# Kernel tuning notes

Measured on AMD Instinct MI355X. Metric: run time of the kernel, lower is better.

Reference implementation:

```python
import jax, jax.numpy as jnp
import numpy as np

MASK_FILL = -99999.0  # value used by masked_fill_ in the torch source


def setup_inputs() -> dict:
    key = jax.random.key(0)
    k1, k2, k3, k4, k5, k6, k7 = jax.random.split(key, 7)
    B, S, H = 8, 2048, 1024
    query = jax.random.normal(k1, (B, S, H), dtype=jnp.float32)
    key_t = jax.random.normal(k2, (B, S, H), dtype=jnp.float32)
    value = jax.random.normal(k3, (B, S, H), dtype=jnp.float32)
    mask = jax.random.randint(k4, (B, S), 0, 2, dtype=jnp.int32)
    s = 1.0 / np.sqrt(H)
    Wq = jax.random.uniform(k5, (H, H), dtype=jnp.float32, minval=-s, maxval=s)
    Wk = jax.random.uniform(k6, (H, H), dtype=jnp.float32, minval=-s, maxval=s)
    Wv = jax.random.uniform(k7, (H, H), dtype=jnp.float32, minval=-s, maxval=s)
    return {"query": query, "key": key_t, "value": value,
            "Wq": Wq, "Wk": Wk, "Wv": Wv, "mask": mask}


def reference(query, key, value, Wq, Wk, Wv, mask):
    # Linear(h,h,bias=False): y = x @ W.T
    q = jnp.einsum('bsh,oh->bso', query, Wq)
    k = jnp.einsum('bsh,oh->bso', key, Wk)
    v = jnp.einsum('bsh,oh->bso', value, Wv)
    # score[b,i,j] = q[b,i,:] . k[b,j,:]  (NO 1/sqrt(d) scaling in source)
    score = jnp.einsum('bqh,bkh->bqk', q, k)
    # mask: [B, S_k] -> [B, 1, S_k]; positions where mask==0 get MASK_FILL
    m = mask[:, None, :]
    score = jnp.where(m == 0, jnp.float32(MASK_FILL), score)
    attn = jax.nn.softmax(score, axis=-1)
    context = jnp.einsum('bqk,bkh->bqh', attn, v)
    return context
```

## Files before the change

kernel.cpp:

```cpp
#include <hip/hip_runtime.h>
#include <hip/hip_fp16.h>
#include <math.h>

typedef _Float16 f16;
typedef _Float16 f16x4 __attribute__((ext_vector_type(4)));
typedef _Float16 f16x8 __attribute__((ext_vector_type(8)));
typedef float f32x4 __attribute__((ext_vector_type(4)));
typedef float f32x4e __attribute__((ext_vector_type(4)));

#define GLOAD_LDS16(g, l)                                                                  \
    __builtin_amdgcn_global_load_lds((const __attribute__((address_space(1))) void*)(g),   \
                                     (__attribute__((address_space(3))) void*)(l), 16, 0, 0)

__global__ __launch_bounds__(256) void cast3_kernel(const float* __restrict__ s0,
                                                    const float* __restrict__ s1,
                                                    const float* __restrict__ s2,
                                                    f16* d0, f16* d1, f16* d2, int n16each)
{
    const int z = blockIdx.z;
    const float* src = (z == 0) ? s0 : (z == 1) ? s1 : s2;
    f16* dst = (z == 0) ? d0 : (z == 1) ? d1 : d2;
    const int stride = gridDim.x * blockDim.x;
    for (int i = blockIdx.x * blockDim.x + threadIdx.x; i < n16each; i += stride) {
        const f32x4e* sp = (const f32x4e*)(src + (long long)i * 16);
        f32x4e a = __builtin_nontemporal_load(sp + 0);
        f32x4e b = __builtin_nontemporal_load(sp + 1);
        f32x4e c = __builtin_nontemporal_load(sp + 2);
        f32x4e d4 = __builtin_nontemporal_load(sp + 3);
        f16x8 lo = {(f16)a[0], (f16)a[1], (f16)a[2], (f16)a[3],
                    (f16)b[0], (f16)b[1], (f16)b[2], (f16)b[3]};
        f16x8 hi = {(f16)c[0], (f16)c[1], (f16)c[2], (f16)c[3],
                    (f16)d4[0], (f16)d4[1], (f16)d4[2], (f16)d4[3]};
        f16x8* dp = (f16x8*)(dst + (long long)i * 16);
        dp[0] = lo;
        dp[1] = hi;
    }
}

__global__ __launch_bounds__(256) void transcast_w_kernel(const float* __restrict__ Wq,
                                                          const float* __restrict__ Wk,
                                                          f16* __restrict__ dA,
                                                          f16* __restrict__ dB)
{
    __shared__ f16 tile[64][72];
    const float* src = blockIdx.z ? Wk : Wq;
    f16* dst = blockIdx.z ? dB : dA;
    const int h0 = blockIdx.x * 64, o0 = blockIdx.y * 64;
    const int t = threadIdx.x;
    const int r = t >> 2, c = (t & 3) * 16;
    const float* sp = src + (long long)(o0 + r) * 1024 + h0 + c;
    float4 v0 = *(const float4*)(sp + 0);
    float4 v1 = *(const float4*)(sp + 4);
    float4 v2 = *(const float4*)(sp + 8);
    float4 v3 = *(const float4*)(sp + 12);
    *(f16x4*)&tile[r][c]      = (f16x4){(f16)v0.x, (f16)v0.y, (f16)v0.z, (f16)v0.w};
    *(f16x4*)&tile[r][c + 4]  = (f16x4){(f16)v1.x, (f16)v1.y, (f16)v1.z, (f16)v1.w};
    *(f16x4*)&tile[r][c + 8]  = (f16x4){(f16)v2.x, (f16)v2.y, (f16)v2.z, (f16)v2.w};
    *(f16x4*)&tile[r][c + 12] = (f16x4){(f16)v3.x, (f16)v3.y, (f16)v3.z, (f16)v3.w};
    __syncthreads();
    f16 buf[16];
#pragma unroll
    for (int j = 0; j < 16; j++) buf[j] = tile[c + j][r];
    f16* dp = dst + (long long)(h0 + r) * 1024 + o0 + c;
    *(f16x8*)(dp)     = *(f16x8*)&buf[0];
    *(f16x8*)(dp + 8) = *(f16x8*)&buf[8];
}

template <int OUTF16, int TRANSC>
__global__ __launch_bounds__(512, 2) void gemm_nt_k(
    const f16* __restrict__ Ab, const f16* __restrict__ Bb, void* __restrict__ Cb,
    int K, int lda, int ldb, int ldc,
    long long sA, long long sB, long long sC, int gx)
{
    __shared__ __align__(16) f16 smem[256 * 64 + 128 * 64];
    constexpr int B_OFF_E = 256 * 64;
    constexpr int B_OFF_B = B_OFF_E * 2;

    const int nwg = gridDim.x;
    const int swz = (blockIdx.x & 7) * (nwg >> 3) + (blockIdx.x >> 3);
    const int bx = swz % gx, by = swz / gx;

    const int z = blockIdx.z;
    const char* pA = (const char*)(Ab + z * sA + (long long)by * 256 * lda);
    const char* pB = (const char*)(Bb + z * sB + (long long)bx * 128 * ldb);
    const long long lda2 = (long long)lda * 2, ldb2 = (long long)ldb * 2;

    const int tid = threadIdx.x;
    const int w = tid >> 6, l = tid & 63;
    const int wr = w >> 1, wc = w & 1;

    f32x4 acc[4][4];
#pragma unroll
    for (int i = 0; i < 4; i++)
#pragma unroll
        for (int j = 0; j < 4; j++) acc[i][j] = (f32x4){0.f, 0.f, 0.f, 0.f};

    const int lr = l & 15;
    const int lkb = (l >> 4) * 16;

#define FRAG_A16(row, kbyte)                                                              \
    (*(const f16x8*)((const char*)&smem[0] + ((row) * 128) + ((kbyte) ^ (((row) & 7) << 4))))
#define FRAG_B(row, kbyte)                                                                \
    (*(const f16x8*)((const char*)&smem[0] + B_OFF_B + ((row) * 128) + ((kbyte) ^ (((row) & 7) << 4))))

    const int nt = K >> 6;
    for (int t = 0; t < nt; ++t) {
        const long long kb = (long long)t * 128;
#pragma unroll
        for (int i = 0; i < 4; i++) {
            const int c = i * 512 + tid;
            const int row = c >> 3;
            const int col = ((c & 7) * 16) ^ ((row & 7) << 4);
            GLOAD_LDS16(pA + (long long)row * lda2 + kb + col, &smem[(long long)c * 8]);
        }
#pragma unroll
        for (int i = 0; i < 2; i++) {
            const int c = i * 512 + tid;
            const int row = c >> 3;
            const int col = ((c & 7) * 16) ^ ((row & 7) << 4);
            GLOAD_LDS16(pB + (long long)row * ldb2 + kb + col, &smem[B_OFF_E + (long long)c * 8]);
        }
        __syncthreads();

        f16x8 bf[4][2], af[4][2];
#pragma unroll
        for (int fc = 0; fc < 4; fc++)
#pragma unroll
            for (int ks = 0; ks < 2; ks++)
                bf[fc][ks] = FRAG_B(wc * 64 + fc * 16 + lr, ks * 64 + lkb);
#pragma unroll
        for (int fq = 0; fq < 4; fq++)
#pragma unroll
            for (int ks = 0; ks < 2; ks++)
                af[fq][ks] = FRAG_A16(wr * 64 + fq * 16 + lr, ks * 64 + lkb);

#pragma unroll
        for (int fq = 0; fq < 4; fq++)
#pragma unroll
            for (int fc = 0; fc < 4; fc++)
#pragma unroll
                for (int ks = 0; ks < 2; ks++)
                    acc[fq][fc] = __builtin_amdgcn_mfma_f32_16x16x32_f16(
                        af[fq][ks], bf[fc][ks], acc[fq][fc], 0, 0, 0);

        __syncthreads();
    }
#undef FRAG_A16
#undef FRAG_B

    const int row_l = (l >> 4) * 4;
    const long long gr0 = (long long)by * 256 + wr * 64;
    const int gc0 = bx * 128 + wc * 64;

    if (TRANSC) {
        const long long blk_r0 = (long long)by * 256;
        const int b = (int)(blk_r0 >> 11);
        const int s_base = (int)(blk_r0 & 2047);
        f16* vTp = (f16*)Cb + (long long)b * 1024 * 2048;
#pragma unroll
        for (int h = 0; h < 2; h++) {
            __syncthreads();
            if ((wr >> 1) == h) {
                const int s64 = (wr & 1) * 64;
#pragma unroll
                for (int fq = 0; fq < 4; fq++)
#pragma unroll
                    for (int fc = 0; fc < 4; fc++)
#pragma unroll
                        for (int i = 0; i < 4; i++)
                            smem[(wc * 64 + fc * 16 + lr) * 136 + s64 + fq * 16 + row_l + i] =
                                (f16)acc[fq][fc][i];
            }
            __syncthreads();
#pragma unroll
            for (int j = 0; j < 4; j++) {
                const int c = j * 512 + tid;
                const int o = c >> 4, s8 = (c & 15) * 8;
                f16x8 vv = *(const f16x8*)&smem[o * 136 + s8];
                *(f16x8*)&vTp[((long long)(bx * 128 + o)) * 2048 + s_base + h * 128 + s8] = vv;
            }
        }
    } else if (OUTF16) {
        f16* C = (f16*)Cb + z * sC;
#pragma unroll
        for (int fq = 0; fq < 4; fq++)
#pragma unroll
            for (int fc = 0; fc < 4; fc++)
#pragma unroll
                for (int i = 0; i < 4; i++)
                    C[(gr0 + fq * 16 + row_l + i) * ldc + gc0 + fc * 16 + lr] = (f16)acc[fq][fc][i];
    } else {
        float* C = (float*)Cb + z * sC;
#pragma unroll
        for (int fq = 0; fq < 4; fq++)
#pragma unroll
            for (int fc = 0; fc < 4; fc++)
#pragma unroll
                for (int i = 0; i < 4; i++)
                    C[(gr0 + fq * 16 + row_l + i) * ldc + gc0 + fc * 16 + lr] = acc[fq][fc][i];
    }
}

__device__ __forceinline__ float wred_max(float v) {
#pragma unroll
    for (int o = 32; o > 0; o >>= 1) v = fmaxf(v, __shfl_xor(v, o));
    return v;
}
__device__ __forceinline__ float wred_sum(float v) {
#pragma unroll
    for (int o = 32; o > 0; o >>= 1) v += __shfl_xor(v, o);
    return v;
}

__global__ __launch_bounds__(256) void softmax_kernel(f16* __restrict__ Sm, const int* __restrict__ mask)
{
    const long long row = blockIdx.x;
    const int b = (int)(row >> 11);
    f16* Srow = Sm + row * 2048;
    const int* mrow = mask + b * 2048;
    const int t = threadIdx.x;
    const int w = t >> 6, l = t & 63;

    f16x8 sv = *(const f16x8*)(Srow + t * 8);
    int4 m0 = *(const int4*)(mrow + t * 8);
    int4 m1 = *(const int4*)(mrow + t * 8 + 4);
    int mk[8] = {m0.x, m0.y, m0.z, m0.w, m1.x, m1.y, m1.z, m1.w};
    float v[8];
#pragma unroll
    for (int j = 0; j < 8; j++) v[j] = (float)sv[j];

    float mx = -INFINITY;
#pragma unroll
    for (int j = 0; j < 8; j++) if (mk[j]) mx = fmaxf(mx, v[j]);
    mx = wred_max(mx);
    __shared__ float redm[4], reds[4];
    if (l == 0) redm[w] = mx;
    __syncthreads();
    mx = fmaxf(fmaxf(redm[0], redm[1]), fmaxf(redm[2], redm[3]));

    if (mx == -INFINITY) {
        const f16 u = (f16)(1.0f / 2048.0f);
        f16x8 pv;
#pragma unroll
        for (int j = 0; j < 8; j++) pv[j] = u;
        *(f16x8*)(Srow + t * 8) = pv;
        return;
    }

    float e[8];
    float s = 0.f;
#pragma unroll
    for (int j = 0; j < 8; j++) { e[j] = mk[j] ? expf(v[j] - mx) : 0.f; s += e[j]; }
    s = wred_sum(s);
    if (l == 0) reds[w] = s;
    __syncthreads();
    s = reds[0] + reds[1] + reds[2] + reds[3];
    const float inv = 1.0f / s;
    f16x8 pv;
#pragma unroll
    for (int j = 0; j < 8; j++) pv[j] = (f16)(e[j] * inv);
    *(f16x8*)(Srow + t * 8) = pv;
}

extern "C" void kernel_launch(void* const* d_in, const int* in_sizes, int n_in,
                              void* d_out, int out_size, void* d_ws, size_t ws_size,
                              hipStream_t stream)
{
    const float* query = (const float*)d_in[0];
    const float* keyi  = (const float*)d_in[1];
    const float* value = (const float*)d_in[2];
    const float* Wq    = (const float*)d_in[3];
    const float* Wk    = (const float*)d_in[4];
    const float* Wv    = (const float*)d_in[5];
    const int*   mask  = (const int*)d_in[6];
    float* out = (float*)d_out;

    const long long SH = (long long)8 * 2048 * 1024;
    f16* slot0 = (f16*)d_ws;
    f16* slot1 = slot0 + SH;
    f16* slot2 = slot0 + 2 * SH;
    f16* slot3 = slot0 + 3 * SH;
    f16* slot4 = slot0 + 4 * SH;
    const long long M1 = 1024 * 1024;
    f16* whA = slot1;
    f16* whB = slot1 + M1;
    f16* whC = slot1 + 2 * M1;
    f16* whD = slot1 + 3 * M1;
    f16* Pb  = slot0;

    const int n16x = (int)(SH / 16);
    const int n16w = (int)(M1 / 16);
    const long long zero = 0;

    transcast_w_kernel<<<dim3(16, 16, 2), 256, 0, stream>>>(Wq, Wk, whA, whB);
    cast3_kernel<<<dim3(64, 1, 1), 256, 0, stream>>>(Wv, Wv, Wv, whC, whC, whC, n16w);
    gemm_nt_k<1, 0><<<dim3(32, 1, 1), 512, 0, stream>>>(
        whA, whB, (void*)whD, 1024, 1024, 1024, 1024, zero, zero, zero, 8);
    cast3_kernel<<<dim3(1024, 1, 2), 256, 0, stream>>>(keyi, value, value, slot0, slot3, slot3, n16x);
    gemm_nt_k<1, 1><<<dim3(512, 1, 1), 512, 0, stream>>>(
        slot3, whC, (void*)slot4, 1024, 1024, 1024, 2048, zero, zero, zero, 8);
    gemm_nt_k<1, 0><<<dim3(512, 1, 1), 512, 0, stream>>>(
        slot0, whD, (void*)slot3, 1024, 1024, 1024, 1024, zero, zero, zero, 8);
    cast3_kernel<<<dim3(1024, 1, 1), 256, 0, stream>>>(query, query, query, slot2, slot2, slot2, n16x);
    gemm_nt_k<1, 0><<<dim3(128, 1, 8), 512, 0, stream>>>(
        slot2, slot3, (void*)Pb, 1024, 1024, 1024, 2048,
        (long long)2048 * 1024, (long long)2048 * 1024, (long long)2048 * 2048, 16);
    softmax_kernel<<<dim3(16384), 256, 0, stream>>>(Pb, mask);
    gemm_nt_k<0, 0><<<dim3(64, 1, 8), 512, 0, stream>>>(
        Pb, slot4, (void*)out, 2048, 2048, 2048, 1024,
        (long long)2048 * 2048, (long long)1024 * 2048, (long long)2048 * 1024, 8);
}
```

Measured before the change: 327.6 us.

## Fuse weight prep launches and overlap Wq·Wk product GEMM with input casts

Merges the Wq/Wk transpose-cast and the Wv cast into a single launch. The small 1024x1024 weight-product GEMM is folded into the key/value cast kernel as extra blocks so it runs alongside the bulk casts, where before it was a separate launch using only 32 workgroups. Cast kernels switch from grid-stride loops to one 16-element chunk per thread, and the final fp32 output stores become nontemporal. The cost removed is the launch gaps and the poorly occupied small GEMM. In exchange, the embedded GEMM is a simple single-buffered 128x128 tile loop.

```diff
diff --git a/kernel.cpp b/kernel.cpp
--- a/kernel.cpp
+++ b/kernel.cpp
@@ -12,41 +12,48 @@
     __builtin_amdgcn_global_load_lds((const __attribute__((address_space(1))) void*)(g),   \
                                      (__attribute__((address_space(3))) void*)(l), 16, 0, 0)
 
-__global__ __launch_bounds__(256) void cast3_kernel(const float* __restrict__ s0,
-                                                    const float* __restrict__ s1,
-                                                    const float* __restrict__ s2,
-                                                    f16* d0, f16* d1, f16* d2, int n16each)
-{
+__device__ __forceinline__ void cast16(const float* __restrict__ src, f16* __restrict__ dst,
+                                       long long i)
+{
+    const f32x4e* sp = (const f32x4e*)(src + i * 16);
+    f32x4e a = __builtin_nontemporal_load(sp + 0);
+    f32x4e b = __builtin_nontemporal_load(sp + 1);
+    f32x4e c = __builtin_nontemporal_load(sp + 2);
+    f32x4e d4 = __builtin_nontemporal_load(sp + 3);
+    f16x8 lo = {(f16)a[0], (f16)a[1], (f16)a[2], (f16)a[3],
+                (f16)b[0], (f16)b[1], (f16)b[2], (f16)b[3]};
+    f16x8 hi = {(f16)c[0], (f16)c[1], (f16)c[2], (f16)c[3],
+                (f16)d4[0], (f16)d4[1], (f16)d4[2], (f16)d4[3]};
+    f16x8* dp = (f16x8*)(dst + i * 16);
+    dp[0] = lo;
+    dp[1] = hi;
+}
+
+__global__ __launch_bounds__(256) void cast1_kernel(const float* __restrict__ src,
+                                                    f16* __restrict__ dst, int n16)
+{
+    const int i = blockIdx.x * blockDim.x + threadIdx.x;
+    if (i < n16) cast16(src, dst, i);
+}
+
+__global__ __launch_bounds__(256) void prep_w_kernel(const float* __restrict__ Wq,
+                                                     const float* __restrict__ Wk,
+                                                     const float* __restrict__ Wv,
+                                                     f16* __restrict__ dA,
+                                                     f16* __restrict__ dB,
+                                                     f16* __restrict__ dC)
+{
+    __shared__ f16 tile[64][72];
     const int z = blockIdx.z;
-    const float* src = (z == 0) ? s0 : (z == 1) ? s1 : s2;
-    f16* dst = (z == 0) ? d0 : (z == 1) ? d1 : d2;
-    const int stride = gridDim.x * blockDim.x;
-    for (int i = blockIdx.x * blockDim.x + threadIdx.x; i < n16each; i += stride) {
-        const f32x4e* sp = (const f32x4e*)(src + (long long)i * 16);
-        f32x4e a = __builtin_nontemporal_load(sp + 0);
-        f32x4e b = __builtin_nontemporal_load(sp + 1);
-        f32x4e c = __builtin_nontemporal_load(sp + 2);
-        f32x4e d4 = __builtin_nontemporal_load(sp + 3);
-        f16x8 lo = {(f16)a[0], (f16)a[1], (f16)a[2], (f16)a[3],
-                    (f16)b[0], (f16)b[1], (f16)b[2], (f16)b[3]};
-        f16x8 hi = {(f16)c[0], (f16)c[1], (f16)c[2], (f16)c[3],
-                    (f16)d4[0], (f16)d4[1], (f16)d4[2], (f16)d4[3]};
-        f16x8* dp = (f16x8*)(dst + (long long)i * 16);
-        dp[0] = lo;
-        dp[1] = hi;
-    }
-}
-
-__global__ __launch_bounds__(256) void transcast_w_kernel(const float* __restrict__ Wq,
-                                                          const float* __restrict__ Wk,
-                                                          f16* __restrict__ dA,
-                                                          f16* __restrict__ dB)
-{
-    __shared__ f16 tile[64][72];
-    const float* src = blockIdx.z ? Wk : Wq;
-    f16* dst = blockIdx.z ? dB : dA;
+    const int t = threadIdx.x;
+    if (z == 2) {
+        const long long i = (long long)(blockIdx.y * 16 + blockIdx.x) * 256 + t;
+        cast16(Wv, dC, i);
+        return;
+    }
+    const float* src = z ? Wk : Wq;
+    f16* dst = z ? dB : dA;
     const int h0 = blockIdx.x * 64, o0 = blockIdx.y * 64;
-    const int t = threadIdx.x;
     const int r = t >> 2, c = (t & 3) * 16;
     const float* sp = src + (long long)(o0 + r) * 1024 + h0 + c;
     float4 v0 = *(const float4*)(sp + 0);
@@ -66,6 +73,68 @@
     *(f16x8*)(dp + 8) = *(f16x8*)&buf[8];
 }
 
+__global__ __launch_bounds__(256) void fused_cast_m_kernel(
+    const float* __restrict__ Xk, const float* __restrict__ Xv,
+    f16* __restrict__ dXk, f16* __restrict__ dXv,
+    const f16* __restrict__ whA, const f16* __restrict__ whB, f16* __restrict__ whD)
+{
+    __shared__ __align__(16) f16 msmem[128 * 32 * 2];
+    const int z = blockIdx.z;
+    const int tid = threadIdx.x;
+    if (z == 0) { cast16(Xk, dXk, (long long)blockIdx.x * 256 + tid); return; }
+    if (z == 1) { cast16(Xv, dXv, (long long)blockIdx.x * 256 + tid); return; }
+    if (blockIdx.x >= 64) return;
+
+    const int b = blockIdx.x;
+    const int by = b >> 3, bx = b & 7;
+    const char* pA = (const char*)(whA + (long long)by * 128 * 1024);
+    const char* pB = (const char*)(whB + (long long)bx * 128 * 1024);
+    const int w = tid >> 6, l = tid & 63;
+    const int wr = w >> 1, wc = w & 1;
+    f32x4 acc[4][4];
+#pragma unroll
+    for (int i = 0; i < 4; i++)
+#pragma unroll
+        for (int j = 0; j < 4; j++) acc[i][j] = (f32x4){0.f, 0.f, 0.f, 0.f};
+    const int lr = l & 15, lkb = (l >> 4) * 16;
+
+    for (int t = 0; t < 32; ++t) {
+        const long long kb = (long long)t * 64;
+#pragma unroll
+        for (int i = 0; i < 2; i++) {
+            const int c = i * 256 + tid;
+            const int row = c >> 2;
+            const int col = ((c & 3) * 16) ^ ((row & 3) << 4);
+            GLOAD_LDS16(pA + (long long)row * 2048 + kb + col, &msmem[(long long)c * 8]);
+            GLOAD_LDS16(pB + (long long)row * 2048 + kb + col, &msmem[4096 + (long long)c * 8]);
+        }
+        __syncthreads();
+        f16x8 af[4], bf[4];
+#pragma unroll
+        for (int f = 0; f < 4; f++) {
+            const int ra = wr * 64 + f * 16 + lr;
+            const int rb = wc * 64 + f * 16 + lr;
+            af[f] = *(const f16x8*)((const char*)&msmem[0] + ra * 64 + (lkb ^ ((ra & 3) << 4)));
+            bf[f] = *(const f16x8*)((const char*)&msmem[4096] + rb * 64 + (lkb ^ ((rb & 3) << 4)));
+        }
+#pragma unroll
+        for (int fq = 0; fq < 4; fq++)
+#pragma unroll
+            for (int fc = 0; fc < 4; fc++)
+                acc[fq][fc] = __builtin_amdgcn_mfma_f32_16x16x32_f16(af[fq], bf[fc], acc[fq][fc], 0, 0, 0);
+        __syncthreads();
+    }
+    const int rowl = (l >> 4) * 4;
+#pragma unroll
+    for (int fq = 0; fq < 4; fq++)
+#pragma unroll
+        for (int fc = 0; fc < 4; fc++)
+#pragma unroll
+            for (int i = 0; i < 4; i++)
+                whD[(long long)(by * 128 + wr * 64 + fq * 16 + rowl + i) * 1024 +
+                    bx * 128 + wc * 64 + fc * 16 + lr] = (f16)acc[fq][fc][i];
+}
+
 template <int OUTF16, int TRANSC>
 __global__ __launch_bounds__(512, 2) void gemm_nt_k(
     const f16* __restrict__ Ab, const f16* __restrict__ Bb, void* __restrict__ Cb,
@@ -197,7 +266,9 @@
             for (int fc = 0; fc < 4; fc++)
 #pragma unroll
                 for (int i = 0; i < 4; i++)
-                    C[(gr0 + fq * 16 + row_l + i) * ldc + gc0 + fc * 16 + lr] = acc[fq][fc][i];
+                    __builtin_nontemporal_store(
+                        acc[fq][fc][i],
+                        &C[(gr0 + fq * 16 + row_l + i) * ldc + gc0 + fc * 16 + lr]);
     }
 }
 
@@ -289,19 +360,16 @@
     f16* Pb  = slot0;
 
     const int n16x = (int)(SH / 16);
-    const int n16w = (int)(M1 / 16);
     const long long zero = 0;
 
-    transcast_w_kernel<<<dim3(16, 16, 2), 256, 0, stream>>>(Wq, Wk, whA, whB);
-    cast3_kernel<<<dim3(64, 1, 1), 256, 0, stream>>>(Wv, Wv, Wv, whC, whC, whC, n16w);
-    gemm_nt_k<1, 0><<<dim3(32, 1, 1), 512, 0, stream>>>(
-        whA, whB, (void*)whD, 1024, 1024, 1024, 1024, zero, zero, zero, 8);
-    cast3_kernel<<<dim3(1024, 1, 2), 256, 0, stream>>>(keyi, value, value, slot0, slot3, slot3, n16x);
+    prep_w_kernel<<<dim3(16, 16, 3), 256, 0, stream>>>(Wq, Wk, Wv, whA, whB, whC);
+    fused_cast_m_kernel<<<dim3(4096, 1, 3), 256, 0, stream>>>(
+        keyi, value, slot0, slot3, whA, whB, whD);
     gemm_nt_k<1, 1><<<dim3(512, 1, 1), 512, 0, stream>>>(
         slot3, whC, (void*)slot4, 1024, 1024, 1024, 2048, zero, zero, zero, 8);
     gemm_nt_k<1, 0><<<dim3(512, 1, 1), 512, 0, stream>>>(
         slot0, whD, (void*)slot3, 1024, 1024, 1024, 1024, zero, zero, zero, 8);
-    cast3_kernel<<<dim3(1024, 1, 1), 256, 0, stream>>>(query, query, query, slot2, slot2, slot2, n16x);
+    cast1_kernel<<<dim3(4096), 256, 0, stream>>>(query, slot2, n16x);
     gemm_nt_k<1, 0><<<dim3(128, 1, 8), 512, 0, stream>>>(
         slot2, slot3, (void*)Pb, 1024, 1024, 1024, 2048,
         (long long)2048 * 1024, (long long)2048 * 1024, (long long)2048 * 2048, 16);
```

After: 314.9 us. -3.9%, faster.
